# Kernel optimization log

Hardware: AMD Instinct MI355X
Metric: run time of the kernel (lower is better)

The kernel has to match this reference:

```python
import jax, jax.numpy as jnp
import numpy as np

N_ENT = 100000
N_REL = 500
D = 200  # rank[0]==rank[1]==rank[2]
B = 512


def setup_inputs() -> dict:
    key = jax.random.key(0)
    k1, k2, k3, k4, k5, k6 = jax.random.split(key, 6)
    X_subj = jax.random.randint(k5, (B,), 0, N_ENT)
    X_rel = jax.random.randint(k6, (B,), 0, N_REL)
    X = jnp.stack([X_subj, X_rel], axis=1)  # [B, 2] int
    return {
        "X": X,
        "E1": jax.random.normal(k1, (N_ENT, D), dtype=jnp.float32) * 0.1,
        "R": jax.random.normal(k2, (N_REL, D), dtype=jnp.float32) * 0.1,
        "E2": jax.random.normal(k3, (N_ENT, D), dtype=jnp.float32) * 0.1,
        "W": jax.random.normal(k4, (D, D, D), dtype=jnp.float32) * 0.05,
    }


def reference(X, E1, R, E2, W):
    # sparse one-hot @ dense == direct gather (row select)
    e1 = E1[X[:, 0]]                 # [B, D]
    r = R[X[:, 1]]                   # [B, D]
    # torch: W.view(r.size(1), -1) reshapes (D,D,D) row-major -> (D, D*D),
    # so relation contracts over W's FIRST axis.
    W_mat = jnp.einsum('bi,ijk->bjk', r, W)    # [B, D, D]
    x = jnp.einsum('bj,bjk->bk', e1, W_mat)    # [B, D]
    logits = x @ E2.T                           # [B, N_ENT]
    return jax.nn.sigmoid(logits)
```

## Files before the change

### kernel.cpp

```cpp
#include <hip/hip_runtime.h>
#include <cstdint>
#include <cstddef>

#define DDIM 200
#define KPAD 224
#define BATCH 512
#define NENT 100000
#define KFLAT 40000
#define SPLIT 50
#define CHUNK_K 800
#define K1_BM 64
#define BROW 232

typedef __attribute__((ext_vector_type(8))) short bf16x8;
typedef __attribute__((ext_vector_type(4))) float f32x4;
typedef __attribute__((ext_vector_type(4))) unsigned short u16x4;
typedef unsigned short u16;

__device__ inline u16 f2bf(float f) {
    union { float f; uint32_t u; } v; v.f = f;
    uint32_t u = v.u;
    u += 0x7FFFu + ((u >> 16) & 1u);
    return (u16)(u >> 16);
}
__device__ inline float bf2f(u16 b) {
    union { uint32_t u; float f; } v; v.u = ((uint32_t)b) << 16;
    return v.f;
}

__global__ __launch_bounds__(256) void transpose_w_bf16(
    const float* __restrict__ W, u16* __restrict__ Wt)
{
    __shared__ u16 T[DDIM][72];
    const int tid = threadIdx.x;
    const int ij0 = blockIdx.x * 64;

    for (int l = tid; l < 64 * 50; l += 256) {
        int m = l & 63, c4 = l >> 6;
        f32x4 v = *(const f32x4*)&W[(size_t)(ij0 + m) * DDIM + c4 * 4];
        #pragma unroll
        for (int q = 0; q < 4; ++q) T[c4 * 4 + q][m] = f2bf(v[q]);
    }
    __syncthreads();
    for (int l = tid; l < DDIM * 8; l += 256) {
        int n = l >> 3, g = l & 7;
        *(bf16x8*)&Wt[(size_t)n * KFLAT + ij0 + g * 8] =
            *(const bf16x8*)&T[n][g * 8];
    }
}

__global__ __launch_bounds__(256) void tucker_x_partial(
    const int* __restrict__ X, const float* __restrict__ E1,
    const float* __restrict__ R, const u16* __restrict__ Wt,
    float* __restrict__ x_part)
{
    __shared__ u16   e1_s[K1_BM][DDIM + 2];
    __shared__ float r_s[K1_BM][4];
    __shared__ u16   At[K1_BM][40];
    __shared__ u16   Bt[208][40];

    const int tid = threadIdx.x;
    const int b0 = blockIdx.x * K1_BM;
    const int chunk = blockIdx.y;
    const int i0 = chunk * 4;
    const int kflat0 = chunk * CHUNK_K;

    for (int l = tid; l < K1_BM * 50; l += 256) {
        int m = l / 50, c4 = l - (l / 50) * 50;
        int subj = X[(b0 + m) * 2 + 0];
        f32x4 v = *(const f32x4*)&E1[(size_t)subj * DDIM + c4 * 4];
        u16x4 b;
        b[0] = f2bf(v[0]); b[1] = f2bf(v[1]); b[2] = f2bf(v[2]); b[3] = f2bf(v[3]);
        *(u16x4*)&e1_s[m][c4 * 4] = b;
    }
    if (tid < K1_BM * 4) {
        int m = tid >> 2, q = tid & 3;
        int rel = X[(b0 + m) * 2 + 1];
        r_s[m][q] = R[(size_t)rel * DDIM + i0 + q];
    }
    for (int l = tid; l < 8 * 40; l += 256)
        Bt[200 + l / 40][l % 40] = 0;

    const int wid = tid >> 6, lane = tid & 63;
    const int lr = lane & 15, lq = lane >> 4;

    f32x4 acc[13];
    #pragma unroll
    for (int f = 0; f < 13; ++f)
        #pragma unroll
        for (int q = 0; q < 4; ++q) acc[f][q] = 0.f;

    for (int s = 0; s < CHUNK_K / 32; ++s) {
        __syncthreads();
        {
            int m = tid >> 2, kb = (tid & 3) * 8;
            bf16x8 av;
            #pragma unroll
            for (int e = 0; e < 8; ++e) {
                int kk = s * 32 + kb + e;
                int io = kk / DDIM;
                int j = kk - io * DDIM;
                float v = r_s[m][io] * bf2f(e1_s[m][j]);
                av[e] = (short)f2bf(v);
            }
            *(bf16x8*)&At[m][kb] = av;
        }
        for (int l = tid; l < DDIM * 4; l += 256) {
            int n = l >> 2, g = l & 3;
            *(bf16x8*)&Bt[n][g * 8] =
                *(const bf16x8*)&Wt[(size_t)n * KFLAT + kflat0 + s * 32 + g * 8];
        }
        __syncthreads();
        bf16x8 af = *(const bf16x8*)&At[wid * 16 + lr][lq * 8];
        #pragma unroll
        for (int f = 0; f < 13; ++f) {
            bf16x8 bfr = *(const bf16x8*)&Bt[f * 16 + lr][lq * 8];
            acc[f] = __builtin_amdgcn_mfma_f32_16x16x32_bf16(af, bfr, acc[f], 0, 0, 0);
        }
    }

    float* dst = x_part + ((size_t)chunk * BATCH + b0) * DDIM;
    #pragma unroll
    for (int f = 0; f < 13; ++f) {
        int n = f * 16 + lr;
        if (n < DDIM) {
            #pragma unroll
            for (int r4 = 0; r4 < 4; ++r4) {
                int m = wid * 16 + lq * 4 + r4;
                dst[(size_t)m * DDIM + n] = acc[f][r4];
            }
        }
    }
}

__global__ __launch_bounds__(256) void reduce_x(
    const float* __restrict__ part, u16* __restrict__ xbf)
{
    int id = blockIdx.x * 256 + threadIdx.x;
    if (id < BATCH * KPAD) {
        int b = id / KPAD, c = id - (id / KPAD) * KPAD;
        float s = 0.f;
        if (c < DDIM) {
            #pragma unroll 10
            for (int ch = 0; ch < SPLIT; ++ch)
                s += part[(size_t)ch * BATCH * DDIM + b * DDIM + c];
        }
        xbf[id] = f2bf(s);
    }
}

__global__ __launch_bounds__(512) void logits_sigmoid_mfma(
    const u16* __restrict__ xbf, const float* __restrict__ E2,
    float* __restrict__ out)
{
    __shared__ __align__(16) unsigned char lds_pool[8 * 16 * 72 * 4];
    u16   (*Bs)[BROW]   = (u16 (*)[BROW])lds_pool;
    float (*Ts)[16][72] = (float (*)[16][72])lds_pool;

    const int tid = threadIdx.x;
    const int n0 = blockIdx.x * 64;
    const int wid = tid >> 6, lane = tid & 63;
    const int lr = lane & 15, lq = lane >> 4;

    for (int l = tid; l < 64 * 50; l += 512) {
        int row = l / 50, c4 = l - (l / 50) * 50;
        int gn = n0 + row;
        u16x4 bb; bb[0] = 0; bb[1] = 0; bb[2] = 0; bb[3] = 0;
        if (gn < NENT) {
            f32x4 v = *(const f32x4*)&E2[(size_t)gn * DDIM + c4 * 4];
            bb[0] = f2bf(v[0]); bb[1] = f2bf(v[1]);
            bb[2] = f2bf(v[2]); bb[3] = f2bf(v[3]);
        }
        *(u16x4*)&Bs[row][c4 * 4] = bb;
    }
    {
        int row = tid >> 3, g = tid & 7;
        u16x4 z; z[0] = 0; z[1] = 0; z[2] = 0; z[3] = 0;
        *(u16x4*)&Bs[row][200 + g * 4] = z;
    }
    __syncthreads();

    f32x4 acc[4][4];
    #pragma unroll
    for (int fm = 0; fm < 4; ++fm)
        #pragma unroll
        for (int fn = 0; fn < 4; ++fn)
            #pragma unroll
            for (int q = 0; q < 4; ++q) acc[fm][fn][q] = 0.f;

    #pragma unroll
    for (int s = 0; s < 7; ++s) {
        bf16x8 af[4];
        #pragma unroll
        for (int fm = 0; fm < 4; ++fm) {
            int row = wid * 64 + fm * 16 + lr;
            af[fm] = *(const bf16x8*)&xbf[row * KPAD + s * 32 + lq * 8];
        }
        bf16x8 bfr[4];
        #pragma unroll
        for (int fn = 0; fn < 4; ++fn)
            bfr[fn] = *(const bf16x8*)&Bs[fn * 16 + lr][s * 32 + lq * 8];
        #pragma unroll
        for (int fm = 0; fm < 4; ++fm)
            #pragma unroll
            for (int fn = 0; fn < 4; ++fn)
                acc[fm][fn] = __builtin_amdgcn_mfma_f32_16x16x32_bf16(
                    af[fm], bfr[fn], acc[fm][fn], 0, 0, 0);
    }

    __syncthreads();

    #pragma unroll
    for (int fm = 0; fm < 4; ++fm) {
        int gm0 = wid * 64 + fm * 16;
        #pragma unroll
        for (int fn = 0; fn < 4; ++fn)
            #pragma unroll
            for (int r4 = 0; r4 < 4; ++r4)
                Ts[wid][lq * 4 + r4][fn * 16 + lr] = acc[fm][fn][r4];
        #pragma unroll
        for (int rr = 0; rr < 4; ++rr) {
            int row = rr * 4 + lq;
            f32x4 v = *(const f32x4*)&Ts[wid][row][lr * 4];
            f32x4 o;
            #pragma unroll
            for (int q = 0; q < 4; ++q)
                o[q] = __builtin_amdgcn_rcpf(1.0f + __expf(-v[q]));
            int gn = n0 + lr * 4;
            if (gn < NENT)
                *(f32x4*)&out[(size_t)(gm0 + row) * NENT + gn] = o;
        }
    }
}

extern "C" void kernel_launch(void* const* d_in, const int* in_sizes, int n_in,
                              void* d_out, int out_size, void* d_ws, size_t ws_size,
                              hipStream_t stream) {
    const int*   X  = (const int*)d_in[0];
    const float* E1 = (const float*)d_in[1];
    const float* R  = (const float*)d_in[2];
    const float* E2 = (const float*)d_in[3];
    const float* W  = (const float*)d_in[4];
    float* out = (float*)d_out;

    float* x_part = (float*)d_ws;
    u16*   xbf    = (u16*)(x_part + (size_t)SPLIT * BATCH * DDIM);
    u16*   Wt     = xbf + (size_t)BATCH * KPAD;

    transpose_w_bf16<<<KFLAT / 64, 256, 0, stream>>>(W, Wt);
    tucker_x_partial<<<dim3(BATCH / K1_BM, SPLIT), 256, 0, stream>>>(
        X, E1, R, Wt, x_part);
    reduce_x<<<dim3((BATCH * KPAD + 255) / 256), 256, 0, stream>>>(x_part, xbf);
    logits_sigmoid_mfma<<<dim3((NENT + 63) / 64), 512, 0, stream>>>(xbf, E2, out);
}
```

Before: 176.5 us.

## Retile logits GEMM to 128x256 blocks with wide row stores and nontemporal writes

Changes the logits kernel from 64 entities x 512 batch rows per block to 256 entities x 128 batch rows, with a 2x4 warp grid over a 2D launch. The epilogue goes through shared memory so each half-block writes contiguous 1 KB row segments, and the output uses nontemporal stores. The aim is longer coalesced writes of the 200 MB output and less cache pollution from it. In exchange each E2 tile is now reloaded and converted by four blocks instead of one, and the epilogue adds block-wide barriers.

After: 200.9 us. +13.8%, slower.

```diff
diff --git a/kernel.cpp b/kernel.cpp
--- a/kernel.cpp
+++ b/kernel.cpp
@@ -10,7 +10,10 @@
 #define SPLIT 50
 #define CHUNK_K 800
 #define K1_BM 64
+#define K2_BM 128
+#define K2_BN 256
 #define BROW 232
+#define TS_W 260
 
 typedef __attribute__((ext_vector_type(8))) short bf16x8;
 typedef __attribute__((ext_vector_type(4))) float f32x4;
@@ -153,16 +156,17 @@
     const u16* __restrict__ xbf, const float* __restrict__ E2,
     float* __restrict__ out)
 {
-    __shared__ __align__(16) unsigned char lds_pool[8 * 16 * 72 * 4];
-    u16   (*Bs)[BROW]   = (u16 (*)[BROW])lds_pool;
-    float (*Ts)[16][72] = (float (*)[16][72])lds_pool;
+    __shared__ __align__(16) unsigned char pool[K2_BN * BROW * 2];
+    u16 (*Bs)[BROW] = (u16 (*)[BROW])pool;
 
     const int tid = threadIdx.x;
-    const int n0 = blockIdx.x * 64;
+    const int n0 = blockIdx.x * K2_BN;
+    const int m0 = blockIdx.y * K2_BM;
     const int wid = tid >> 6, lane = tid & 63;
+    const int wm = wid >> 2, wn = wid & 3;
     const int lr = lane & 15, lq = lane >> 4;
 
-    for (int l = tid; l < 64 * 50; l += 512) {
+    for (int l = tid; l < K2_BN * 50; l += 512) {
         int row = l / 50, c4 = l - (l / 50) * 50;
         int gn = n0 + row;
         u16x4 bb; bb[0] = 0; bb[1] = 0; bb[2] = 0; bb[3] = 0;
@@ -173,8 +177,8 @@
         }
         *(u16x4*)&Bs[row][c4 * 4] = bb;
     }
-    {
-        int row = tid >> 3, g = tid & 7;
+    for (int l = tid; l < K2_BN * 8; l += 512) {
+        int row = l >> 3, g = l & 7;
         u16x4 z; z[0] = 0; z[1] = 0; z[2] = 0; z[3] = 0;
         *(u16x4*)&Bs[row][200 + g * 4] = z;
     }
@@ -193,13 +197,13 @@
         bf16x8 af[4];
         #pragma unroll
         for (int fm = 0; fm < 4; ++fm) {
-            int row = wid * 64 + fm * 16 + lr;
+            int row = m0 + wm * 64 + fm * 16 + lr;
             af[fm] = *(const bf16x8*)&xbf[row * KPAD + s * 32 + lq * 8];
         }
         bf16x8 bfr[4];
         #pragma unroll
         for (int fn = 0; fn < 4; ++fn)
-            bfr[fn] = *(const bf16x8*)&Bs[fn * 16 + lr][s * 32 + lq * 8];
+            bfr[fn] = *(const bf16x8*)&Bs[wn * 64 + fn * 16 + lr][s * 32 + lq * 8];
         #pragma unroll
         for (int fm = 0; fm < 4; ++fm)
             #pragma unroll
@@ -210,26 +214,32 @@
 
     __syncthreads();
 
+    float (*Ts)[TS_W] = (float (*)[TS_W])(pool + (size_t)wm * (16 * TS_W * 4));
+    const int hrow = (tid & 255) >> 4;
+    const int li   = tid & 15;
+
     #pragma unroll
     for (int fm = 0; fm < 4; ++fm) {
-        int gm0 = wid * 64 + fm * 16;
         #pragma unroll
         for (int fn = 0; fn < 4; ++fn)
             #pragma unroll
             for (int r4 = 0; r4 < 4; ++r4)
-                Ts[wid][lq * 4 + r4][fn * 16 + lr] = acc[fm][fn][r4];
-        #pragma unroll
-        for (int rr = 0; rr < 4; ++rr) {
-            int row = rr * 4 + lq;
-            f32x4 v = *(const f32x4*)&Ts[wid][row][lr * 4];
+                Ts[lq * 4 + r4][wn * 64 + fn * 16 + lr] = acc[fm][fn][r4];
+        __syncthreads();
+        int gm = m0 + wm * 64 + fm * 16 + hrow;
+        #pragma unroll
+        for (int q = 0; q < 4; ++q) {
+            f32x4 v = *(const f32x4*)&Ts[hrow][li * 4 + q * 64];
             f32x4 o;
             #pragma unroll
-            for (int q = 0; q < 4; ++q)
-                o[q] = __builtin_amdgcn_rcpf(1.0f + __expf(-v[q]));
-            int gn = n0 + lr * 4;
+            for (int j = 0; j < 4; ++j)
+                o[j] = __builtin_amdgcn_rcpf(1.0f + __expf(-v[j]));
+            int gn = n0 + li * 4 + q * 64;
             if (gn < NENT)
-                *(f32x4*)&out[(size_t)(gm0 + row) * NENT + gn] = o;
-        }
+                __builtin_nontemporal_store(o,
+                    (f32x4*)&out[(size_t)gm * NENT + gn]);
+        }
+        __syncthreads();
     }
 }
 
@@ -251,5 +261,6 @@
     tucker_x_partial<<<dim3(BATCH / K1_BM, SPLIT), 256, 0, stream>>>(
         X, E1, R, Wt, x_part);
     reduce_x<<<dim3((BATCH * KPAD + 255) / 256), 256, 0, stream>>>(x_part, xbf);
-    logits_sigmoid_mfma<<<dim3((NENT + 63) / 64), 512, 0, stream>>>(xbf, E2, out);
-}
+    logits_sigmoid_mfma<<<dim3((NENT + K2_BN - 1) / K2_BN, BATCH / K2_BM),
+                          512, 0, stream>>>(xbf, E2, out);
+}
```
